# Kernel tuning notes

Measured on AMD Instinct MI355X. Metric: run time of the kernel, lower is better.

The kernel has to match this reference:

```python
import jax, jax.numpy as jnp
import numpy as np

T = 4096   # reference sequence length (concatenated virtual samples)
L = 4096   # modality sequence length
D_Q = 64   # reference feature dim
D_QK = 128 # projected query/key dim (before add_one -> 129)
D_V = 128  # value dim
N_IDS = 8  # number of virtual samples encoded in idx


def setup_inputs() -> dict:
    key = jax.random.key(0)
    ks = jax.random.split(key, 20)
    inp = {}
    inp['ref_data'] = jax.random.normal(ks[0], (1, 1, T, D_Q), jnp.float32)
    inp['ref_time'] = jnp.sort(jax.random.uniform(ks[1], (1, T), jnp.float32), axis=-1)
    inp['ref_idx'] = jnp.sort(jax.random.randint(ks[2], (T,), 0, N_IDS))
    inp['m1_data'] = jax.random.normal(ks[3], (1, 1, L, 130), jnp.float32)
    inp['m1_time'] = jnp.sort(jax.random.uniform(ks[4], (1, L), jnp.float32), axis=-1)
    inp['m1_idx'] = jnp.sort(jax.random.randint(ks[5], (L,), 0, N_IDS))
    inp['m2_data'] = jax.random.normal(ks[6], (1, 1, L, 66), jnp.float32)
    inp['m2_time'] = jnp.sort(jax.random.uniform(ks[7], (1, L), jnp.float32), axis=-1)
    inp['m2_idx'] = jnp.sort(jax.random.randint(ks[8], (L,), 0, N_IDS))
    s = 0.05
    inp['Wq'] = jax.random.normal(ks[9], (D_Q, D_QK), jnp.float32) * s
    inp['bq'] = jnp.zeros((D_QK,), jnp.float32)
    inp['Wk1'] = jax.random.normal(ks[10], (1, D_QK), jnp.float32) * s
    inp['bk1'] = jnp.zeros((D_QK,), jnp.float32)
    inp['Wv1'] = jax.random.normal(ks[11], (128, D_V), jnp.float32) * s
    inp['bv1'] = jnp.zeros((D_V,), jnp.float32)
    inp['Wk2'] = jax.random.normal(ks[12], (1, D_QK), jnp.float32) * s
    inp['bk2'] = jnp.zeros((D_QK,), jnp.float32)
    inp['Wv2'] = jax.random.normal(ks[13], (64, D_V), jnp.float32) * s
    inp['bv2'] = jnp.zeros((D_V,), jnp.float32)
    inp['log_tau1'] = jnp.zeros((), jnp.float32)  # log(init_tau=1)
    inp['log_tau2'] = jnp.zeros((), jnp.float32)
    return inp


def _add_one_q(x):  # add_one(x, dim=1): append ones on last axis
    return jnp.concatenate([x, jnp.ones(x.shape[:-1] + (1,), x.dtype)], axis=-1)


def _feat_k(x):  # add_one(x, dim=0): [ones, -x]
    return jnp.concatenate([jnp.ones(x.shape[:-1] + (1,), x.dtype), -x], axis=-1)


def _uni_attn(Q, mdata, q_t, kv_t, q_idx, kv_idx, Wk, bk, Wv, bv, log_tau):
    # qk_type='time': keys from last feature (timestamp), values from data[..., :-2]
    K = _feat_k(mdata[..., -1:] @ Wk + bk)          # (1,1,L,d_qk+1)
    V = mdata[..., :-2] @ Wv + bv                   # (1,1,L,d_v)
    tau = jnp.exp(log_tau)
    # gaussian weight: -(Q.K)^2 / tau
    A = -jnp.square(jnp.einsum('nhtc,nhlc->nhtl', Q, K)) / tau  # (1,1,T,L)
    causal = (q_t[:, :, None] >= kv_t[:, None, :]).astype(Q.dtype)[:, None]  # (1,1,T,L)
    neg_inf = jnp.array(-jnp.inf, Q.dtype)
    bm = jnp.where(q_idx[None, :, None] == kv_idx[None, None, :], jnp.zeros((), Q.dtype), neg_inf)  # (1,T,L)
    fully_masked = jnp.all(jnp.isneginf(bm), axis=-1, keepdims=True)
    safe = jnp.where(fully_masked, jnp.zeros((), Q.dtype), bm)[:, None]  # (1,1,T,L)
    A = jax.nn.softmax(A * causal + safe, axis=-1) * causal
    return jnp.einsum('nhtl,nhlc->nhtc', A, V)      # (1,1,T,d_v)


def reference(ref_data, ref_time, m1_data, m1_time, m2_data, m2_time,
              Wq, bq, Wk1, bk1, Wv1, bv1, Wk2, bk2, Wv2, bv2,
              log_tau1, log_tau2, ref_idx, m1_idx, m2_idx):
    Q = _add_one_q(ref_data @ Wq + bq)  # (1,1,T,d_qk+1)
    y1 = _uni_attn(Q, m1_data, ref_time, m1_time, ref_idx, m1_idx, Wk1, bk1, Wv1, bv1, log_tau1)
    y2 = _uni_attn(Q, m2_data, ref_time, m2_time, ref_idx, m2_idx, Wk2, bk2, Wv2, bv2, log_tau2)
    return jnp.concatenate([y1, y2], axis=-1)  # (1,1,T,2*d_v)
```

## Files before the change

kernel.cpp:

```cpp
#include <hip/hip_runtime.h>
#include <hip/hip_bf16.h>

#define TQ 4096
#define LK 4096
#define QT 16
#define NSPLIT 4
#define CHJ 32
#define PB 32
#define PQ (TQ / PB)

template<bool BF> __device__ __forceinline__ float ld(const void* p, int i);
template<> __device__ __forceinline__ float ld<true>(const void* p, int i) {
    return __bfloat162float(((const __hip_bfloat16*)p)[i]);
}
template<> __device__ __forceinline__ float ld<false>(const void* p, int i) {
    return ((const float*)p)[i];
}
template<bool BF> __device__ __forceinline__ float2 ld2(const void* p, int i);
template<> __device__ __forceinline__ float2 ld2<false>(const void* p, int i) {
    return *(const float2*)((const float*)p + i);
}
template<> __device__ __forceinline__ float2 ld2<true>(const void* p, int i) {
    float2 r; r.x = ld<true>(p, i); r.y = ld<true>(p, i + 1); return r;
}
template<bool BF> __device__ __forceinline__ float4 ld4(const void* p, int i);
template<> __device__ __forceinline__ float4 ld4<false>(const void* p, int i) {
    return *(const float4*)((const float*)p + i);
}
template<> __device__ __forceinline__ float4 ld4<true>(const void* p, int i) {
    float4 r; r.x = ld<true>(p, i); r.y = ld<true>(p, i + 1);
    r.z = ld<true>(p, i + 2); r.w = ld<true>(p, i + 3); return r;
}
template<bool BF> __device__ __forceinline__ void st4(void* p, int i, float4 v);
template<> __device__ __forceinline__ void st4<true>(void* p, int i, float4 v) {
    __hip_bfloat16* o = (__hip_bfloat16*)p + i;
    o[0] = __float2bfloat16(v.x); o[1] = __float2bfloat16(v.y);
    o[2] = __float2bfloat16(v.z); o[3] = __float2bfloat16(v.w);
}
template<> __device__ __forceinline__ void st4<false>(void* p, int i, float4 v) {
    *(float4*)((float*)p + i) = v;
}

__device__ __forceinline__ bool sniff_bf16(const void* ref_time) {
    const int lane = threadIdx.x & 63;
    bool ok = true;
    if (lane < 32) {
        float v = __bfloat162float(((const __hip_bfloat16*)ref_time)[2 * lane]);
        ok = (v >= 0.0f) && (v <= 1.0f);
    }
    return __ballot(ok) == ~0ULL;
}

__device__ int lb_int(const int* arr, int n, int key) {
    int lo = 0, hi = n;
    while (lo < hi) { int mid = (lo + hi) >> 1; if (arr[mid] < key) lo = mid + 1; else hi = mid; }
    return lo;
}
__device__ int ub_int(const int* arr, int n, int key) {
    int lo = 0, hi = n;
    while (lo < hi) { int mid = (lo + hi) >> 1; if (arr[mid] <= key) lo = mid + 1; else hi = mid; }
    return lo;
}

template<bool BF>
__device__ void prep_body(
    const void* ref_data, const void* ref_time, const int* ref_idx,
    const void* m1_time, const int* m1_idx, const void* m2_time, const int* m2_idx,
    const void* Wq, const void* bq,
    const void* Wk1, const void* bk1, const void* Wk2, const void* bk2,
    float* alpha1, float* beta1, float* alpha2, float* beta2,
    int* c1, int* s1, int* e1, int* c2, int* s2, int* e2)
{
    __shared__ float ut[64][4];
    __shared__ float cst[4];
    __shared__ int tabs[4][8];

    const int tid = threadIdx.x;
    const int i = tid >> 2, r = tid & 3;

    {
        const void* w = (r == 0) ? Wk1 : (r == 1) ? bk1 : (r == 2) ? Wk2 : bk2;
        const bool isA = (r & 1);
        float acc = isA ? ld<BF>(Wq, i * 128) : 0.0f;
        const float sgn = isA ? -1.0f : 1.0f;
        #pragma unroll 4
        for (int d = 1; d < 128; ++d)
            acc = fmaf(sgn * ld<BF>(Wq, i * 128 + d), ld<BF>(w, d - 1), acc);
        ut[i][r] = acc;
    }
    if (tid < 4) {
        const void* w = (tid == 0) ? Wk1 : (tid == 1) ? bk1 : (tid == 2) ? Wk2 : bk2;
        const bool isA = (tid & 1);
        float c = isA ? ld<BF>(bq, 0) : 0.0f;
        const float sgn = isA ? -1.0f : 1.0f;
        #pragma unroll 4
        for (int d = 1; d < 128; ++d)
            c = fmaf(sgn * ld<BF>(bq, d), ld<BF>(w, d - 1), c);
        c += sgn * ld<BF>(w, 127);
        cst[tid] = c;
    }
    if (tid >= 4 && tid < 36) {
        const int k = tid - 4;
        const int sid = k & 7, rest = k >> 3;
        const int modk = rest & 1, kind = rest >> 1;
        const int* arr = modk ? m2_idx : m1_idx;
        tabs[modk * 2 + kind][sid] = kind ? ub_int(arr, LK, sid) : lb_int(arr, LK, sid);
    }
    __syncthreads();

    const int q = tid & 127;
    const int t = blockIdx.x * PQ + q;
    if (tid < 128) {
        float4 acc = {cst[0], cst[1], cst[2], cst[3]};
        #pragma unroll
        for (int ii = 0; ii < 64; ii += 4) {
            const float4 rv = ld4<BF>(ref_data, t * 64 + ii);
            const float4 u0 = *(const float4*)ut[ii + 0];
            const float4 u1 = *(const float4*)ut[ii + 1];
            const float4 u2 = *(const float4*)ut[ii + 2];
            const float4 u3 = *(const float4*)ut[ii + 3];
            acc.x = fmaf(rv.x, u0.x, fmaf(rv.y, u1.x, fmaf(rv.z, u2.x, fmaf(rv.w, u3.x, acc.x))));
            acc.y = fmaf(rv.x, u0.y, fmaf(rv.y, u1.y, fmaf(rv.z, u2.y, fmaf(rv.w, u3.y, acc.y))));
            acc.z = fmaf(rv.x, u0.z, fmaf(rv.y, u1.z, fmaf(rv.z, u2.z, fmaf(rv.w, u3.z, acc.z))));
            acc.w = fmaf(rv.x, u0.w, fmaf(rv.y, u1.w, fmaf(rv.z, u2.w, fmaf(rv.w, u3.w, acc.w))));
        }
        beta1[t] = acc.x; alpha1[t] = acc.y;
        beta2[t] = acc.z; alpha2[t] = acc.w;
    } else {
        const float qt = ld<BF>(ref_time, t);
        const int g = ref_idx[t];
        int lo1 = 0, hi1 = LK, lo2 = 0, hi2 = LK;
        #pragma unroll
        for (int it = 0; it < 13; ++it) {
            const int mA = min((lo1 + hi1) >> 1, LK - 1);
            const int mB = min((lo2 + hi2) >> 1, LK - 1);
            const float v1 = ld<BF>(m1_time, mA);
            const float v2 = ld<BF>(m2_time, mB);
            if (lo1 < hi1) { if (v1 <= qt) lo1 = mA + 1; else hi1 = mA; }
            if (lo2 < hi2) { if (v2 <= qt) lo2 = mB + 1; else hi2 = mB; }
        }
        c1[t] = lo1; c2[t] = lo2;
        s1[t] = tabs[0][g]; e1[t] = tabs[1][g];
        s2[t] = tabs[2][g]; e2[t] = tabs[3][g];
    }
}

__global__ __launch_bounds__(256) void prep_kernel(
    const void* ref_data, const void* ref_time, const int* ref_idx,
    const void* m1_time, const int* m1_idx, const void* m2_time, const int* m2_idx,
    const void* Wq, const void* bq,
    const void* Wk1, const void* bk1, const void* Wk2, const void* bk2,
    float* alpha1, float* beta1, float* alpha2, float* beta2,
    int* c1, int* s1, int* e1, int* c2, int* s2, int* e2)
{
    if (sniff_bf16(ref_time))
        prep_body<true>(ref_data, ref_time, ref_idx, m1_time, m1_idx, m2_time, m2_idx,
                        Wq, bq, Wk1, bk1, Wk2, bk2,
                        alpha1, beta1, alpha2, beta2, c1, s1, e1, c2, s2, e2);
    else
        prep_body<false>(ref_data, ref_time, ref_idx, m1_time, m1_idx, m2_time, m2_idx,
                         Wq, bq, Wk1, bk1, Wk2, bk2,
                         alpha1, beta1, alpha2, beta2, c1, s1, e1, c2, s2, e2);
}

template<bool BF, int K, int DM>
__device__ void vproj_wave(const void* md, const void* Wv, const void* bv,
                           float* V, float* X, int rows0)
{
    const int lane = threadIdx.x & 63;
    const int cT = lane & 31;
    const int rG = lane >> 5;
    const int r0 = rows0 + rG * 4;
    const int c4 = cT * 4;

    const float4 bb = ld4<BF>(bv, c4);
    float4 acc[4] = {bb, bb, bb, bb};

    #pragma unroll 2
    for (int k = 0; k < K; k += 4) {
        const float4 w0 = ld4<BF>(Wv, (k + 0) * 128 + c4);
        const float4 w1 = ld4<BF>(Wv, (k + 1) * 128 + c4);
        const float4 w2 = ld4<BF>(Wv, (k + 2) * 128 + c4);
        const float4 w3 = ld4<BF>(Wv, (k + 3) * 128 + c4);
        float2 alo[4], ahi[4];
        #pragma unroll
        for (int r = 0; r < 4; ++r) {
            alo[r] = ld2<BF>(md, (r0 + r) * DM + k);
            ahi[r] = ld2<BF>(md, (r0 + r) * DM + k + 2);
        }
        #pragma unroll
        for (int r = 0; r < 4; ++r) {
            acc[r].x = fmaf(alo[r].x, w0.x, fmaf(alo[r].y, w1.x, fmaf(ahi[r].x, w2.x, fmaf(ahi[r].y, w3.x, acc[r].x))));
            acc[r].y = fmaf(alo[r].x, w0.y, fmaf(alo[r].y, w1.y, fmaf(ahi[r].x, w2.y, fmaf(ahi[r].y, w3.y, acc[r].y))));
            acc[r].z = fmaf(alo[r].x, w0.z, fmaf(alo[r].y, w1.z, fmaf(ahi[r].x, w2.z, fmaf(ahi[r].y, w3.z, acc[r].z))));
            acc[r].w = fmaf(alo[r].x, w0.w, fmaf(alo[r].y, w1.w, fmaf(ahi[r].x, w2.w, fmaf(ahi[r].y, w3.w, acc[r].w))));
        }
    }
    #pragma unroll
    for (int r = 0; r < 4; ++r)
        *(float4*)&V[(size_t)(r0 + r) * 128 + c4] = acc[r];
    if (rG == 0 && cT < 8)
        X[rows0 + cT] = ld<BF>(md, (rows0 + cT) * DM + DM - 1);
}

__global__ __launch_bounds__(64) void vproj_kernel(
    const void* __restrict__ ref_time,
    const void* m1_data, const void* Wv1, const void* bv1,
    const void* m2_data, const void* Wv2, const void* bv2,
    float* V1, float* V2, float* X1, float* X2)
{
    const int rows0 = blockIdx.x * 8;
    const int mod = blockIdx.y;
    const bool bf = sniff_bf16(ref_time);
    if (mod == 0) {
        if (bf) vproj_wave<true, 128, 130>(m1_data, Wv1, bv1, V1, X1, rows0);
        else    vproj_wave<false, 128, 130>(m1_data, Wv1, bv1, V1, X1, rows0);
    } else {
        if (bf) vproj_wave<true, 64, 66>(m2_data, Wv2, bv2, V2, X2, rows0);
        else    vproj_wave<false, 64, 66>(m2_data, Wv2, bv2, V2, X2, rows0);
    }
}

__global__ __launch_bounds__(128) void attn_kernel(
    const void* __restrict__ ref_time,
    const float* __restrict__ alpha1, const float* __restrict__ beta1,
    const float* __restrict__ alpha2, const float* __restrict__ beta2,
    const int* __restrict__ c1, const int* __restrict__ s1, const int* __restrict__ e1,
    const int* __restrict__ c2, const int* __restrict__ s2, const int* __restrict__ e2,
    const float* __restrict__ V1, const float* __restrict__ V2,
    const float* __restrict__ X1, const float* __restrict__ X2,
    const void* log_tau1, const void* log_tau2,
    float* __restrict__ Opart, float* __restrict__ Zpart)
{
    __shared__ float sW[2][CHJ * QT];
    __shared__ float sO[QT * 128];
    __shared__ float sZm[QT];

    const int tid = threadIdx.x;
    const int wid = tid >> 6, lane = tid & 63;
    const int t0 = blockIdx.x * QT, zb = blockIdx.y, mod = blockIdx.z;

    const bool bf = sniff_bf16(ref_time);
    const float* alpha = mod ? alpha2 : alpha1;
    const float* beta  = mod ? beta2  : beta1;
    const int* cA = mod ? c2 : c1;
    const int* sA = mod ? s2 : s1;
    const int* eA = mod ? e2 : e1;
    const float* V = mod ? V2 : V1;
    const float* X = mod ? X2 : X1;
    const void* ltp = mod ? log_tau2 : log_tau1;
    const float scale = __expf(-(bf ? ld<true>(ltp, 0) : ld<false>(ltp, 0)));

    const int q = lane & 15;
    const int t = t0 + q;
    int s = sA[t], e = eA[t];
    const int c = cA[t];
    if (s == e) { s = 0; e = LK; }
    const int cm = min(c, e);
    const float al = alpha[t], be = beta[t];

    int es = (cm > s) ? s : 0x7fffffff;
    int ec = (cm > s) ? cm : 0;
    #pragma unroll
    for (int o = 1; o < 64; o <<= 1) {
        es = min(es, __shfl_xor(es, o));
        ec = max(ec, __shfl_xor(ec, o));
    }
    int jlo = es, jhi = ec;
    if (jlo > jhi) { jlo = 0; jhi = 0; }
    const int W = jhi - jlo;
    const int chunk = (W + NSPLIT * 2 - 1) / (NSPLIT * 2);
    const int sub = zb * 2 + wid;
    const int lo = jlo + sub * chunk;
    int hi = min(jhi, lo + chunk); if (hi < lo) hi = lo;
    const int nch = (chunk + CHJ - 1) / CHJ;

    const int cT = lane & 31, qG = lane >> 5;
    const int jj = lane >> 4;
    float4 acc[8] = {{0,0,0,0},{0,0,0,0},{0,0,0,0},{0,0,0,0},
                     {0,0,0,0},{0,0,0,0},{0,0,0,0},{0,0,0,0}};
    float zacc = 0.0f;
    float* myW = sW[wid];
    const float4* __restrict__ Vg = (const float4*)V;

    for (int ci = 0; ci < nch; ++ci) {
        const int base = lo + ci * CHJ;
        const int jm = min(CHJ, hi - base);
        if (jm > 0) {
            #pragma unroll
            for (int p = 0; p < 8; ++p) {
                const int jr = jj + p * 4;
                const int j = base + jr;
                const bool ok = (jr < jm) && (j >= s) && (j < cm);
                const float x = X[min(j, LK - 1)];
                const float qk = fmaf(-be, x, al);
                const float w = ok ? __expf(-(qk * qk) * scale) : 0.0f;
                myW[jr * QT + q] = w;
                zacc += w;
            }
        }
        __syncthreads();
        if (jm > 0) {
            #pragma unroll 4
            for (int j = 0; j < jm; ++j) {
                const float4 v = Vg[(base + j) * 32 + cT];
                const float4* wv = (const float4*)&myW[j * QT + qG * 8];
                const float4 wA = wv[0], wB = wv[1];
                acc[0].x = fmaf(wA.x, v.x, acc[0].x); acc[0].y = fmaf(wA.x, v.y, acc[0].y);
                acc[0].z = fmaf(wA.x, v.z, acc[0].z); acc[0].w = fmaf(wA.x, v.w, acc[0].w);
                acc[1].x = fmaf(wA.y, v.x, acc[1].x); acc[1].y = fmaf(wA.y, v.y, acc[1].y);
                acc[1].z = fmaf(wA.y, v.z, acc[1].z); acc[1].w = fmaf(wA.y, v.w, acc[1].w);
                acc[2].x = fmaf(wA.z, v.x, acc[2].x); acc[2].y = fmaf(wA.z, v.y, acc[2].y);
                acc[2].z = fmaf(wA.z, v.z, acc[2].z); acc[2].w = fmaf(wA.z, v.w, acc[2].w);
                acc[3].x = fmaf(wA.w, v.x, acc[3].x); acc[3].y = fmaf(wA.w, v.y, acc[3].y);
                acc[3].z = fmaf(wA.w, v.z, acc[3].z); acc[3].w = fmaf(wA.w, v.w, acc[3].w);
                acc[4].x = fmaf(wB.x, v.x, acc[4].x); acc[4].y = fmaf(wB.x, v.y, acc[4].y);
                acc[4].z = fmaf(wB.x, v.z, acc[4].z); acc[4].w = fmaf(wB.x, v.w, acc[4].w);
                acc[5].x = fmaf(wB.y, v.x, acc[5].x); acc[5].y = fmaf(wB.y, v.y, acc[5].y);
                acc[5].z = fmaf(wB.y, v.z, acc[5].z); acc[5].w = fmaf(wB.y, v.w, acc[5].w);
                acc[6].x = fmaf(wB.z, v.x, acc[6].x); acc[6].y = fmaf(wB.z, v.y, acc[6].y);
                acc[6].z = fmaf(wB.z, v.z, acc[6].z); acc[6].w = fmaf(wB.z, v.w, acc[6].w);
                acc[7].x = fmaf(wB.w, v.x, acc[7].x); acc[7].y = fmaf(wB.w, v.y, acc[7].y);
                acc[7].z = fmaf(wB.w, v.z, acc[7].z); acc[7].w = fmaf(wB.w, v.w, acc[7].w);
            }
        }
        __syncthreads();
    }

    float z = zacc;
    z += __shfl_xor(z, 16);
    z += __shfl_xor(z, 32);

    const int part = zb * 2 + mod;
    if (wid == 0) {
        #pragma unroll
        for (int r = 0; r < 8; ++r)
            *(float4*)&sO[(qG * 8 + r) * 128 + cT * 4] = acc[r];
        if (lane < 16) sZm[lane] = z;
    }
    __syncthreads();
    if (wid == 1) {
        float4* Og = (float4*)Opart;
        #pragma unroll
        for (int r = 0; r < 8; ++r) {
            const float4 o0 = *(const float4*)&sO[(qG * 8 + r) * 128 + cT * 4];
            float4 o = acc[r];
            o.x += o0.x; o.y += o0.y; o.z += o0.z; o.w += o0.w;
            Og[((size_t)(part << 12) + (t0 + qG * 8 + r)) * 32 + cT] = o;
        }
        if (lane < 16) Zpart[(part << 12) + t0 + lane] = z + sZm[lane];
    }
}

__global__ __launch_bounds__(256) void finish_kernel(
    const void* __restrict__ ref_time,
    const int* __restrict__ c1, const int* __restrict__ s1, const int* __restrict__ e1,
    const int* __restrict__ c2, const int* __restrict__ s2, const int* __restrict__ e2,
    const float* __restrict__ Zpart, const float* __restrict__ Opart,
    void* __restrict__ out)
{
    const bool bf = sniff_bf16(ref_time);
    const int idx = blockIdx.x * 256 + threadIdx.x;
    const int t = idx >> 6;
    const int rem = idx & 63;
    const int mod = rem >> 5;
    const int c4 = rem & 31;

    const int* cA = mod ? c2 : c1;
    const int* sA = mod ? s2 : s1;
    const int* eA = mod ? e2 : e1;
    int s = sA[t], e = eA[t];
    const int c = cA[t];
    if (s == e) { s = 0; e = LK; }
    const int nnc = (e > c) ? (e - max(s, c)) : 0;

    float Z = (float)nnc;
    float4 o = {0, 0, 0, 0};
    const float4* Og = (const float4*)Opart;
    #pragma unroll
    for (int zb = 0; zb < NSPLIT; ++zb) {
        const int part = zb * 2 + mod;
        Z += Zpart[(part << 12) + t];
        const float4 p = Og[((size_t)(part << 12) + t) * 32 + c4];
        o.x += p.x; o.y += p.y; o.z += p.z; o.w += p.w;
    }
    const float inv = 1.0f / fmaxf(Z, 1.0e-20f);
    o.x *= inv; o.y *= inv; o.z *= inv; o.w *= inv;
    if (bf) st4<true>(out, t * 256 + mod * 128 + c4 * 4, o);
    else    st4<false>(out, t * 256 + mod * 128 + c4 * 4, o);
}

extern "C" void kernel_launch(void* const* d_in, const int* in_sizes, int n_in,
                              void* d_out, int out_size, void* d_ws, size_t ws_size,
                              hipStream_t stream)
{
    const void* ref_data = d_in[0];
    const void* ref_time = d_in[1];
    const int*  ref_idx  = (const int*)d_in[2];
    const void* m1_data  = d_in[3];
    const void* m1_time  = d_in[4];
    const int*  m1_idx   = (const int*)d_in[5];
    const void* m2_data  = d_in[6];
    const void* m2_time  = d_in[7];
    const int*  m2_idx   = (const int*)d_in[8];
    const void* Wq  = d_in[9];
    const void* bq  = d_in[10];
    const void* Wk1 = d_in[11];
    const void* bk1 = d_in[12];
    const void* Wv1 = d_in[13];
    const void* bv1 = d_in[14];
    const void* Wk2 = d_in[15];
    const void* bk2 = d_in[16];
    const void* Wv2 = d_in[17];
    const void* bv2 = d_in[18];
    const void* log_tau1 = d_in[19];
    const void* log_tau2 = d_in[20];

    float* ws = (float*)d_ws;
    float* alpha1 = ws + 0 * TQ;
    float* beta1  = ws + 1 * TQ;
    float* alpha2 = ws + 2 * TQ;
    float* beta2  = ws + 3 * TQ;
    int*   c1 = (int*)(ws + 4 * TQ);
    int*   c2 = (int*)(ws + 5 * TQ);
    int*   s1 = (int*)(ws + 6 * TQ);
    int*   e1 = (int*)(ws + 7 * TQ);
    int*   s2 = (int*)(ws + 8 * TQ);
    int*   e2 = (int*)(ws + 9 * TQ);
    float* X1 = ws + 10 * TQ;
    float* X2 = ws + 11 * TQ;
    float* V1 = ws + 12 * TQ;
    float* V2 = V1 + (size_t)LK * 128;
    float* Zpart = V2 + (size_t)LK * 128;
    float* Opart = Zpart + 8 * TQ;

    prep_kernel<<<dim3(PB), dim3(256), 0, stream>>>(
        ref_data, ref_time, ref_idx, m1_time, m1_idx, m2_time, m2_idx,
        Wq, bq, Wk1, bk1, Wk2, bk2,
        alpha1, beta1, alpha2, beta2, c1, s1, e1, c2, s2, e2);

    vproj_kernel<<<dim3(LK / 8, 2), dim3(64), 0, stream>>>(
        ref_time, m1_data, Wv1, bv1, m2_data, Wv2, bv2, V1, V2, X1, X2);

    attn_kernel<<<dim3(TQ / QT, NSPLIT, 2), dim3(128), 0, stream>>>(
        ref_time, alpha1, beta1, alpha2, beta2, c1, s1, e1, c2, s2, e2,
        V1, V2, X1, X2, log_tau1, log_tau2, Opart, Zpart);

    finish_kernel<<<dim3(TQ * 2 * 32 / 256), dim3(256), 0, stream>>>(
        ref_time, c1, s1, e1, c2, s2, e2, Zpart, Opart, (void*)d_out);
}
```

Before: 179.3 us.

## Split attention per wave, drop block syncs, widen key split and shrink vproj tiles

The attention kernel now makes each wave own an independent key sub-range and write its own partial output. This removes both __syncthreads per chunk and the shared-memory reduction between the two waves, relying on s_waitcnt lgkmcnt for intra-wave LDS ordering. NSPLIT doubles to 8 (16 partials per query, reduced in finish_kernel) and CHJ halves to 16. The value projection uses 4 rows per block instead of 8 for more blocks. The cost is more partial-buffer traffic and a larger final reduction.

```diff
diff --git a/kernel.cpp b/kernel.cpp
--- a/kernel.cpp
+++ b/kernel.cpp
@@ -4,8 +4,9 @@
 #define TQ 4096
 #define LK 4096
 #define QT 16
-#define NSPLIT 4
-#define CHJ 32
+#define NSPLIT 8
+#define NSUB (NSPLIT * 2)
+#define CHJ 16
 #define PB 32
 #define PQ (TQ / PB)
 
@@ -170,26 +171,26 @@
     const int lane = threadIdx.x & 63;
     const int cT = lane & 31;
     const int rG = lane >> 5;
-    const int r0 = rows0 + rG * 4;
+    const int r0 = rows0 + rG * 2;
     const int c4 = cT * 4;
 
     const float4 bb = ld4<BF>(bv, c4);
-    float4 acc[4] = {bb, bb, bb, bb};
-
-    #pragma unroll 2
+    float4 acc[2] = {bb, bb};
+
+    #pragma unroll 4
     for (int k = 0; k < K; k += 4) {
         const float4 w0 = ld4<BF>(Wv, (k + 0) * 128 + c4);
         const float4 w1 = ld4<BF>(Wv, (k + 1) * 128 + c4);
         const float4 w2 = ld4<BF>(Wv, (k + 2) * 128 + c4);
         const float4 w3 = ld4<BF>(Wv, (k + 3) * 128 + c4);
-        float2 alo[4], ahi[4];
+        float2 alo[2], ahi[2];
         #pragma unroll
-        for (int r = 0; r < 4; ++r) {
+        for (int r = 0; r < 2; ++r) {
             alo[r] = ld2<BF>(md, (r0 + r) * DM + k);
             ahi[r] = ld2<BF>(md, (r0 + r) * DM + k + 2);
         }
         #pragma unroll
-        for (int r = 0; r < 4; ++r) {
+        for (int r = 0; r < 2; ++r) {
             acc[r].x = fmaf(alo[r].x, w0.x, fmaf(alo[r].y, w1.x, fmaf(ahi[r].x, w2.x, fmaf(ahi[r].y, w3.x, acc[r].x))));
             acc[r].y = fmaf(alo[r].x, w0.y, fmaf(alo[r].y, w1.y, fmaf(ahi[r].x, w2.y, fmaf(ahi[r].y, w3.y, acc[r].y))));
             acc[r].z = fmaf(alo[r].x, w0.z, fmaf(alo[r].y, w1.z, fmaf(ahi[r].x, w2.z, fmaf(ahi[r].y, w3.z, acc[r].z))));
@@ -197,9 +198,9 @@
         }
     }
     #pragma unroll
-    for (int r = 0; r < 4; ++r)
+    for (int r = 0; r < 2; ++r)
         *(float4*)&V[(size_t)(r0 + r) * 128 + c4] = acc[r];
-    if (rG == 0 && cT < 8)
+    if (rG == 0 && cT < 4)
         X[rows0 + cT] = ld<BF>(md, (rows0 + cT) * DM + DM - 1);
 }
 
@@ -209,7 +210,7 @@
     const void* m2_data, const void* Wv2, const void* bv2,
     float* V1, float* V2, float* X1, float* X2)
 {
-    const int rows0 = blockIdx.x * 8;
+    const int rows0 = blockIdx.x * 4;
     const int mod = blockIdx.y;
     const bool bf = sniff_bf16(ref_time);
     if (mod == 0) {
@@ -233,8 +234,6 @@
     float* __restrict__ Opart, float* __restrict__ Zpart)
 {
     __shared__ float sW[2][CHJ * QT];
-    __shared__ float sO[QT * 128];
-    __shared__ float sZm[QT];
 
     const int tid = threadIdx.x;
     const int wid = tid >> 6, lane = tid & 63;
@@ -269,11 +268,10 @@
     int jlo = es, jhi = ec;
     if (jlo > jhi) { jlo = 0; jhi = 0; }
     const int W = jhi - jlo;
-    const int chunk = (W + NSPLIT * 2 - 1) / (NSPLIT * 2);
+    const int chunk = (W + NSUB - 1) / NSUB;
     const int sub = zb * 2 + wid;
     const int lo = jlo + sub * chunk;
     int hi = min(jhi, lo + chunk); if (hi < lo) hi = lo;
-    const int nch = (chunk + CHJ - 1) / CHJ;
 
     const int cT = lane & 31, qG = lane >> 5;
     const int jj = lane >> 4;
@@ -283,73 +281,55 @@
     float* myW = sW[wid];
     const float4* __restrict__ Vg = (const float4*)V;
 
-    for (int ci = 0; ci < nch; ++ci) {
-        const int base = lo + ci * CHJ;
+    for (int base = lo; base < hi; base += CHJ) {
         const int jm = min(CHJ, hi - base);
-        if (jm > 0) {
-            #pragma unroll
-            for (int p = 0; p < 8; ++p) {
-                const int jr = jj + p * 4;
-                const int j = base + jr;
-                const bool ok = (jr < jm) && (j >= s) && (j < cm);
-                const float x = X[min(j, LK - 1)];
-                const float qk = fmaf(-be, x, al);
-                const float w = ok ? __expf(-(qk * qk) * scale) : 0.0f;
-                myW[jr * QT + q] = w;
-                zacc += w;
-            }
-        }
-        __syncthreads();
-        if (jm > 0) {
-            #pragma unroll 4
-            for (int j = 0; j < jm; ++j) {
-                const float4 v = Vg[(base + j) * 32 + cT];
-                const float4* wv = (const float4*)&myW[j * QT + qG * 8];
-                const float4 wA = wv[0], wB = wv[1];
-                acc[0].x = fmaf(wA.x, v.x, acc[0].x); acc[0].y = fmaf(wA.x, v.y, acc[0].y);
-                acc[0].z = fmaf(wA.x, v.z, acc[0].z); acc[0].w = fmaf(wA.x, v.w, acc[0].w);
-                acc[1].x = fmaf(wA.y, v.x, acc[1].x); acc[1].y = fmaf(wA.y, v.y, acc[1].y);
-                acc[1].z = fmaf(wA.y, v.z, acc[1].z); acc[1].w = fmaf(wA.y, v.w, acc[1].w);
-                acc[2].x = fmaf(wA.z, v.x, acc[2].x); acc[2].y = fmaf(wA.z, v.y, acc[2].y);
-                acc[2].z = fmaf(wA.z, v.z, acc[2].z); acc[2].w = fmaf(wA.z, v.w, acc[2].w);
-                acc[3].x = fmaf(wA.w, v.x, acc[3].x); acc[3].y = fmaf(wA.w, v.y, acc[3].y);
-                acc[3].z = fmaf(wA.w, v.z, acc[3].z); acc[3].w = fmaf(wA.w, v.w, acc[3].w);
-                acc[4].x = fmaf(wB.x, v.x, acc[4].x); acc[4].y = fmaf(wB.x, v.y, acc[4].y);
-                acc[4].z = fmaf(wB.x, v.z, acc[4].z); acc[4].w = fmaf(wB.x, v.w, acc[4].w);
-                acc[5].x = fmaf(wB.y, v.x, acc[5].x); acc[5].y = fmaf(wB.y, v.y, acc[5].y);
-                acc[5].z = fmaf(wB.y, v.z, acc[5].z); acc[5].w = fmaf(wB.y, v.w, acc[5].w);
-                acc[6].x = fmaf(wB.z, v.x, acc[6].x); acc[6].y = fmaf(wB.z, v.y, acc[6].y);
-                acc[6].z = fmaf(wB.z, v.z, acc[6].z); acc[6].w = fmaf(wB.z, v.w, acc[6].w);
-                acc[7].x = fmaf(wB.w, v.x, acc[7].x); acc[7].y = fmaf(wB.w, v.y, acc[7].y);
-                acc[7].z = fmaf(wB.w, v.z, acc[7].z); acc[7].w = fmaf(wB.w, v.w, acc[7].w);
-            }
-        }
-        __syncthreads();
+        __asm__ volatile("s_waitcnt lgkmcnt(0)" ::: "memory");
+        #pragma unroll
+        for (int p = 0; p < 4; ++p) {
+            const int jr = jj * 4 + p;
+            const int j = base + jr;
+            const bool ok = (jr < jm) && (j >= s) && (j < cm);
+            const float x = X[min(j, LK - 1)];
+            const float qk = fmaf(-be, x, al);
+            const float w = ok ? __expf(-(qk * qk) * scale) : 0.0f;
+            myW[jr * QT + q] = w;
+            zacc += w;
+        }
+        __asm__ volatile("s_waitcnt lgkmcnt(0)" ::: "memory");
+        #pragma unroll 4
+        for (int j = 0; j < jm; ++j) {
+            const float4 v = Vg[(base + j) * 32 + cT];
+            const float4* wv = (const float4*)&myW[j * QT + qG * 8];
+            const float4 wA = wv[0], wB = wv[1];
+            acc[0].x = fmaf(wA.x, v.x, acc[0].x); acc[0].y = fmaf(wA.x, v.y, acc[0].y);
+            acc[0].z = fmaf(wA.x, v.z, acc[0].z); acc[0].w = fmaf(wA.x, v.w, acc[0].w);
+            acc[1].x = fmaf(wA.y, v.x, acc[1].x); acc[1].y = fmaf(wA.y, v.y, acc[1].y);
+            acc[1].z = fmaf(wA.y, v.z, acc[1].z); acc[1].w = fmaf(wA.y, v.w, acc[1].w);
+            acc[2].x = fmaf(wA.z, v.x, acc[2].x); acc[2].y = fmaf(wA.z, v.y, acc[2].y);
+            acc[2].z = fmaf(wA.z, v.z, acc[2].z); acc[2].w = fmaf(wA.z, v.w, acc[2].w);
+            acc[3].x = fmaf(wA.w, v.x, acc[3].x); acc[3].y = fmaf(wA.w, v.y, acc[3].y);
+            acc[3].z = fmaf(wA.w, v.z, acc[3].z); acc[3].w = fmaf(wA.w, v.w, acc[3].w);
+            acc[4].x = fmaf(wB.x, v.x, acc[4].x); acc[4].y = fmaf(wB.x, v.y, acc[4].y);
+            acc[4].z = fmaf(wB.x, v.z, acc[4].z); acc[4].w = fmaf(wB.x, v.w, acc[4].w);
+            acc[5].x = fmaf(wB.y, v.x, acc[5].x); acc[5].y = fmaf(wB.y, v.y, acc[5].y);
+            acc[5].z = fmaf(wB.y, v.z, acc[5].z); acc[5].w = fmaf(wB.y, v.w, acc[5].w);
+            acc[6].x = fmaf(wB.z, v.x, acc[6].x); acc[6].y = fmaf(wB.z, v.y, acc[6].y);
+            acc[6].z = fmaf(wB.z, v.z, acc[6].z); acc[6].w = fmaf(wB.z, v.w, acc[6].w);
+            acc[7].x = fmaf(wB.w, v.x, acc[7].x); acc[7].y = fmaf(wB.w, v.y, acc[7].y);
+            acc[7].z = fmaf(wB.w, v.z, acc[7].z); acc[7].w = fmaf(wB.w, v.w, acc[7].w);
+        }
     }
 
     float z = zacc;
     z += __shfl_xor(z, 16);
     z += __shfl_xor(z, 32);
 
-    const int part = zb * 2 + mod;
-    if (wid == 0) {
-        #pragma unroll
-        for (int r = 0; r < 8; ++r)
-            *(float4*)&sO[(qG * 8 + r) * 128 + cT * 4] = acc[r];
-        if (lane < 16) sZm[lane] = z;
-    }
-    __syncthreads();
-    if (wid == 1) {
-        float4* Og = (float4*)Opart;
-        #pragma unroll
-        for (int r = 0; r < 8; ++r) {
-            const float4 o0 = *(const float4*)&sO[(qG * 8 + r) * 128 + cT * 4];
-            float4 o = acc[r];
-            o.x += o0.x; o.y += o0.y; o.z += o0.z; o.w += o0.w;
-            Og[((size_t)(part << 12) + (t0 + qG * 8 + r)) * 32 + cT] = o;
-        }
-        if (lane < 16) Zpart[(part << 12) + t0 + lane] = z + sZm[lane];
-    }
+    const int part = sub * 2 + mod;
+    float4* Og = (float4*)Opart;
+    #pragma unroll
+    for (int r = 0; r < 8; ++r)
+        Og[((size_t)(part << 12) + (t0 + qG * 8 + r)) * 32 + cT] = acc[r];
+    if (lane < 16) Zpart[(part << 12) + t0 + lane] = z;
 }
 
 __global__ __launch_bounds__(256) void finish_kernel(
@@ -378,8 +358,8 @@
     float4 o = {0, 0, 0, 0};
     const float4* Og = (const float4*)Opart;
     #pragma unroll
-    for (int zb = 0; zb < NSPLIT; ++zb) {
-        const int part = zb * 2 + mod;
+    for (int zi = 0; zi < NSUB; ++zi) {
+        const int part = zi * 2 + mod;
         Z += Zpart[(part << 12) + t];
         const float4 p = Og[((size_t)(part << 12) + t) * 32 + c4];
         o.x += p.x; o.y += p.y; o.z += p.z; o.w += p.w;
@@ -432,14 +412,14 @@
     float* V1 = ws + 12 * TQ;
     float* V2 = V1 + (size_t)LK * 128;
     float* Zpart = V2 + (size_t)LK * 128;
-    float* Opart = Zpart + 8 * TQ;
+    float* Opart = Zpart + 32 * TQ;
 
     prep_kernel<<<dim3(PB), dim3(256), 0, stream>>>(
         ref_data, ref_time, ref_idx, m1_time, m1_idx, m2_time, m2_idx,
         Wq, bq, Wk1, bk1, Wk2, bk2,
         alpha1, beta1, alpha2, beta2, c1, s1, e1, c2, s2, e2);
 
-    vproj_kernel<<<dim3(LK / 8, 2), dim3(64), 0, stream>>>(
+    vproj_kernel<<<dim3(LK / 4, 2), dim3(64), 0, stream>>>(
         ref_time, m1_data, Wv1, bv1, m2_data, Wv2, bv2, V1, V2, X1, X2);
 
     attn_kernel<<<dim3(TQ / QT, NSPLIT, 2), dim3(128), 0, stream>>>(
```

After: 182.3 us. Within noise of the previous version (+1.7%).
